# Kernel tuning notes

Hardware: AMD Instinct MI355X
Metric: run time of the kernel (lower is better)

The kernel has to match this reference:

```python
import jax, jax.numpy as jnp
import numpy as np
import math

N_EMBD = 1024
BATCH = 8
T = 2048
INIT_DECAY = 0.95


def setup_inputs() -> dict:
    key = jax.random.key(0)
    k1, k2 = jax.random.split(key)
    raw_init = math.log(INIT_DECAY / (1.0 - INIT_DECAY))
    x = jax.random.normal(k1, (BATCH, T, N_EMBD), dtype=jnp.float32)
    raw_a = jnp.full((N_EMBD,), raw_init, dtype=jnp.float32)
    B = jax.random.normal(k2, (N_EMBD, N_EMBD), dtype=jnp.float32) * 0.01
    h0 = jnp.zeros((BATCH, N_EMBD), dtype=jnp.float32)
    return {"x": x, "raw_a": raw_a, "B": B, "h0": h0}


def reference(x, raw_a, B, h0):
    # a: [H] diagonal decay in (0,1)
    a = jax.nn.sigmoid(raw_a)
    # Precompute the dense projection for all timesteps at once: u[b,t,h] = x[b,t,:] @ B.T
    u = jnp.einsum('btc,hc->bth', x, B)
    # Diagonal linear recurrence h_t = a * h_{t-1} + u_t via lax.scan over time.
    u_t_first = jnp.swapaxes(u, 0, 1)  # [T, B, H]

    def step(h, u_t):
        h = h * a + u_t
        return h, h

    _, ys = jax.lax.scan(step, h0, u_t_first)  # ys: [T, B, H]
    return jnp.swapaxes(ys, 0, 1)  # [B, T, H]
```

## Files before the change

kernel.cpp:

```cpp
#include <hip/hip_runtime.h>
#include <hip/hip_bf16.h>

using bf16 = __hip_bfloat16;
typedef __attribute__((ext_vector_type(8))) short frag8;
typedef __attribute__((ext_vector_type(4))) float f32x4;

constexpr int   H_   = 1024;
constexpr int   B_   = 8;
constexpr int   T_   = 2048;
constexpr int   K_   = H_;
constexpr int   N_   = H_;
constexpr long  M_   = (long)B_ * T_;
constexpr int   SEG  = 64;
constexpr int   TSEG = T_ / SEG;
constexpr int   NCH  = B_ * H_;
constexpr int   NVC  = NCH / 4;

__device__ __forceinline__ unsigned short f2bf(float f) {
  bf16 b = __float2bfloat16(f);
  return *reinterpret_cast<unsigned short*>(&b);
}

__device__ __forceinline__ float4 fma4(float4 h, float4 a, float4 v) {
  float4 r;
  r.x = fmaf(h.x, a.x, v.x);
  r.y = fmaf(h.y, a.y, v.y);
  r.z = fmaf(h.z, a.z, v.z);
  r.w = fmaf(h.w, a.w, v.w);
  return r;
}

__global__ __launch_bounds__(256) void k_convert(const float* __restrict__ x,
                                                 const float* __restrict__ Bm,
                                                 const float* __restrict__ raw,
                                                 unsigned short* __restrict__ xb,
                                                 unsigned short* __restrict__ Bb,
                                                 float* __restrict__ a_sig) {
  const long NX4 = (M_ * K_) / 4;
  const long NB4 = ((long)N_ * K_) / 4;
  long t = (long)blockIdx.x * 256 + threadIdx.x;
  const float* src; unsigned short* dst;
  if (t < NX4) { src = x; dst = xb; }
  else if (t < NX4 + NB4) { t -= NX4; src = Bm; dst = Bb; }
  else {
    long q = t - NX4 - NB4;
    if (q >= H_ / 4) return;
    float4 v = *reinterpret_cast<const float4*>(raw + q * 4);
    float4 o;
    o.x = 1.0f / (1.0f + expf(-v.x));
    o.y = 1.0f / (1.0f + expf(-v.y));
    o.z = 1.0f / (1.0f + expf(-v.z));
    o.w = 1.0f / (1.0f + expf(-v.w));
    *reinterpret_cast<float4*>(a_sig + q * 4) = o;
    return;
  }
  long i = t * 4;
  float4 v = *reinterpret_cast<const float4*>(src + i);
  short4 o;
  o.x = (short)f2bf(v.x);
  o.y = (short)f2bf(v.y);
  o.z = (short)f2bf(v.z);
  o.w = (short)f2bf(v.w);
  *reinterpret_cast<short4*>(dst + i) = o;
}

#define MEMBAR asm volatile("" ::: "memory")
#define BARR do { MEMBAR; __builtin_amdgcn_s_barrier(); MEMBAR; } while (0)
#define VMW(n) asm volatile("s_waitcnt vmcnt(" #n ")" ::: "memory")
#define GLDS(SRC, DST) __builtin_amdgcn_global_load_lds( \
    (const __attribute__((address_space(1))) void*)(SRC), \
    (__attribute__((address_space(3))) void*)(DST), 16, 0, 0)

__global__ __launch_bounds__(512, 2) void k_gemm(const unsigned short* __restrict__ A,
                                                 const unsigned short* __restrict__ Bb,
                                                 float* __restrict__ C,
                                                 const float* __restrict__ a_sig,
                                                 float* __restrict__ E) {
  __shared__ __align__(16) unsigned short lA[32768];
  __shared__ __align__(16) unsigned short lB[32768];
  const int tid  = threadIdx.x;
  const int wid  = tid >> 6, lane = tid & 63;
  const int wr   = wid >> 2, wc = wid & 3;
  const int quad = lane >> 4, l16 = lane & 15;
  const int sx   = l16 & 7;
  const int bh   = wc >> 1, br = (wc & 1) * 64;
  const int bid  = blockIdx.x;
  const int wgid = (bid & 7) * 32 + (bid >> 3);
  const long m0 = (long)(wgid >> 2) * 256;
  const long n0 = (long)(wgid & 3) * 256;
  const int sgran = (tid & 7) ^ ((tid >> 3) & 7);
  const unsigned short* gA = A  + (m0 + (tid >> 3)) * K_ + sgran * 8;
  const unsigned short* gB = Bb + (n0 + (tid >> 3)) * K_ + sgran * 8;
  unsigned short* sAw = lA + wid * 512;
  unsigned short* sBw = lB + wid * 512;

#define STG_A(d, hf, t) do { \
    GLDS(gA + ((hf) * 128) * K_ + (t) * 64,      sAw + (d) * 16384 + (hf) * 8192); \
    GLDS(gA + ((hf) * 128 + 64) * K_ + (t) * 64, sAw + (d) * 16384 + (hf) * 8192 + 4096); } while (0)
#define STG_B(d, hf, t) do { \
    GLDS(gB + ((hf) * 128) * K_ + (t) * 64,      sBw + (d) * 16384 + (hf) * 8192); \
    GLDS(gB + ((hf) * 128 + 64) * K_ + (t) * 64, sBw + (d) * 16384 + (hf) * 8192 + 4096); } while (0)

  f32x4 acc[8][4];
  #pragma unroll
  for (int i = 0; i < 8; i++)
    #pragma unroll
    for (int j = 0; j < 4; j++) acc[i][j] = f32x4{0.f, 0.f, 0.f, 0.f};

  frag8 aR[4][2];
  frag8 bR[2][2][2];

#define RD_A(d, ih) do { _Pragma("unroll") \
    for (int ii = 0; ii < 4; ii++) { \
      const unsigned short* rp = lA + (d) * 16384 + wr * 8192 + (((ih) * 4 + ii) * 16 + l16) * 64; \
      aR[ii][0] = *(const frag8*)(rp + (quad ^ sx) * 8); \
      aR[ii][1] = *(const frag8*)(rp + ((quad + 4) ^ sx) * 8); } } while (0)
#define RD_B(d, jh) do { _Pragma("unroll") \
    for (int jj = 0; jj < 2; jj++) { \
      const unsigned short* rp = lB + (d) * 16384 + bh * 8192 + (br + ((jh) * 2 + jj) * 16 + l16) * 64; \
      bR[jh][jj][0] = *(const frag8*)(rp + (quad ^ sx) * 8); \
      bR[jh][jj][1] = *(const frag8*)(rp + ((quad + 4) ^ sx) * 8); } } while (0)
#define MMQ(ih, jh) do { __builtin_amdgcn_s_setprio(1); _Pragma("unroll") \
    for (int ii = 0; ii < 4; ii++) { _Pragma("unroll") \
      for (int jj = 0; jj < 2; jj++) { \
        acc[(ih)*4+ii][(jh)*2+jj] = __builtin_amdgcn_mfma_f32_16x16x32_bf16(aR[ii][0], bR[jh][jj][0], acc[(ih)*4+ii][(jh)*2+jj], 0, 0, 0); \
        acc[(ih)*4+ii][(jh)*2+jj] = __builtin_amdgcn_mfma_f32_16x16x32_bf16(aR[ii][1], bR[jh][jj][1], acc[(ih)*4+ii][(jh)*2+jj], 0, 0, 0); } } \
    __builtin_amdgcn_s_setprio(0); } while (0)

  STG_A(0, 0, 0); STG_A(0, 1, 0); STG_B(0, 0, 0); STG_B(0, 1, 0); STG_A(1, 0, 1);
  VMW(2); BARR;

  for (int it = 0; it < 7; ++it) {
    const int to = 2 * it + 1, te2 = 2 * it + 2, to2 = 2 * it + 3;
    RD_A(0, 0); RD_B(0, 0); STG_A(1, 1, to);          BARR; MMQ(0, 0);
    RD_B(0, 1);             STG_B(1, 0, to);          BARR; MMQ(0, 1);
    RD_A(0, 1);             STG_B(1, 1, to);          BARR; MMQ(1, 1);
                            STG_A(0, 0, te2); VMW(2); BARR; MMQ(1, 0);
    RD_A(1, 0); RD_B(1, 0); STG_A(0, 1, te2);         BARR; MMQ(0, 0);
    RD_B(1, 1);             STG_B(0, 0, te2);         BARR; MMQ(0, 1);
    RD_A(1, 1);             STG_B(0, 1, te2);         BARR; MMQ(1, 1);
                            STG_A(1, 0, to2); VMW(2); BARR; MMQ(1, 0);
  }
  RD_A(0, 0); RD_B(0, 0); STG_A(1, 1, 15);         BARR; MMQ(0, 0);
  RD_B(0, 1);             STG_B(1, 0, 15);         BARR; MMQ(0, 1);
  RD_A(0, 1);             STG_B(1, 1, 15);         BARR; MMQ(1, 1);
                                           VMW(0); BARR; MMQ(1, 0);
  RD_A(1, 0); RD_B(1, 0);                          BARR; MMQ(0, 0);
  RD_B(1, 1);                                      BARR; MMQ(0, 1);
  RD_A(1, 1);                                      BARR; MMQ(1, 1);
  MMQ(1, 0);

  #pragma unroll
  for (int i = 0; i < 8; i++)
    #pragma unroll
    for (int j = 0; j < 4; j++) {
      const long r0 = m0 + wr * 128 + i * 16 + quad * 4;
      const long c0 = n0 + wc * 64 + j * 16 + l16;
      #pragma unroll
      for (int r = 0; r < 4; r++)
        C[(r0 + r) * N_ + c0] = acc[i][j][r];
    }

  {
    const int bb = (int)(m0 >> 11);
    const int sB = (int)((m0 & 2047) >> 5);
    #pragma unroll
    for (int j = 0; j < 4; j++) {
      const int c0 = (int)(n0) + wc * 64 + j * 16 + l16;
      const float a  = a_sig[c0];
      const float a2 = a * a, a4 = a2 * a2;
      float p4[8];
      p4[0] = 1.f;
      #pragma unroll
      for (int k = 1; k < 8; k++) p4[k] = p4[k - 1] * a4;
      #pragma unroll
      for (int sp = 0; sp < 4; sp++) {
        const f32x4 v = acc[sp * 2][j];
        const f32x4 w = acc[sp * 2 + 1][j];
        float p0 = ((v[0] * a + v[1]) * a + v[2]) * a + v[3];
        float p1 = ((w[0] * a + w[1]) * a + w[2]) * a + w[3];
        float e = p4[7 - quad] * p0 + p4[3 - quad] * p1;
        e += __shfl_xor(e, 16, 64);
        e += __shfl_xor(e, 32, 64);
        if (quad == 0) {
          const int sg = sB + wr * 4 + sp;
          E[(long)sg * NCH + bb * H_ + c0] = e;
        }
      }
    }
  }
}

__global__ __launch_bounds__(256) void k_scan(float* __restrict__ u,
                                              const float* __restrict__ E,
                                              const float* __restrict__ h0,
                                              const float* __restrict__ a_sig) {
  int g = blockIdx.x * 256 + threadIdx.x;
  int vc = g & (NVC - 1);
  int s  = g >> 11;
  int b  = vc >> 8;
  int h4 = (vc & 255) * 4;
  float4 a = *reinterpret_cast<const float4*>(a_sig + h4);
  float4 aL = a;
  #pragma unroll
  for (int i = 0; i < 5; i++) { aL.x *= aL.x; aL.y *= aL.y; aL.z *= aL.z; aL.w *= aL.w; }
  float4 hs = *reinterpret_cast<const float4*>(h0 + (long)vc * 4);
  int j = 0;
  for (; j + 8 <= s; j += 8) {
    float4 e[8];
    #pragma unroll
    for (int q = 0; q < 8; q++)
      e[q] = *reinterpret_cast<const float4*>(E + (long)(j + q) * NCH + (long)vc * 4);
    #pragma unroll
    for (int q = 0; q < 8; q++)
      hs = fma4(hs, aL, e[q]);
  }
  for (; j < s; ++j) {
    float4 e = *reinterpret_cast<const float4*>(E + (long)j * NCH + (long)vc * 4);
    hs = fma4(hs, aL, e);
  }

  float* base = u + (long)b * T_ * H_ + (long)s * TSEG * H_ + h4;

  float4 v0[8], v1[8];
  #pragma unroll
  for (int jj = 0; jj < 8; jj++)
    v0[jj] = *reinterpret_cast<const float4*>(base + (long)jj * H_);

  #pragma unroll
  for (int t0 = 0; t0 < TSEG; t0 += 8) {
    const bool odd = (t0 >> 3) & 1;
    float4* cur = odd ? v1 : v0;
    float4* nxt = odd ? v0 : v1;
    if (t0 + 8 < TSEG) {
      #pragma unroll
      for (int jj = 0; jj < 8; jj++)
        nxt[jj] = *reinterpret_cast<const float4*>(base + (long)(t0 + 8 + jj) * H_);
    }
    #pragma unroll
    for (int jj = 0; jj < 8; jj++) {
      hs = fma4(hs, a, cur[jj]);
      cur[jj] = hs;
    }
    #pragma unroll
    for (int jj = 0; jj < 8; jj++)
      *reinterpret_cast<float4*>(base + (long)(t0 + jj) * H_) = cur[jj];
  }
}

extern "C" void kernel_launch(void* const* d_in, const int* in_sizes, int n_in,
                              void* d_out, int out_size, void* d_ws, size_t ws_size,
                              hipStream_t stream) {
  const float* x    = (const float*)d_in[0];
  const float* rawa = (const float*)d_in[1];
  const float* Bm   = (const float*)d_in[2];
  const float* h0   = (const float*)d_in[3];
  float* u = (float*)d_out;

  char* w = (char*)d_ws;
  unsigned short* xb = (unsigned short*)w;
  unsigned short* Bb = (unsigned short*)(w + 33554432);
  float* a_sig = (float*)(w + 33554432 + 2097152);
  float* E     = (float*)(w + 33554432 + 2097152 + 4096);

  hipLaunchKernelGGL(k_convert, dim3(17409), dim3(256), 0, stream, x, Bm, rawa, xb, Bb, a_sig);
  hipLaunchKernelGGL(k_gemm, dim3(256), dim3(512), 0, stream, xb, Bb, u, a_sig, E);
  hipLaunchKernelGGL(k_scan, dim3(NVC * SEG / 256), dim3(256), 0, stream, u, E, h0, a_sig);
}
```

Measured before the change: 172.3 us.

## Store GEMM output as bf16 in workspace and scan from bf16 intermediate

The GEMM can now write the projection u as bf16 into a workspace buffer instead of fp32 into the output, and a new scan kernel reads those bf16 values, expands them to fp32 and writes the final states. This halves the intermediate write and read traffic between GEMM and scan, at the cost of bf16 rounding on u before the recurrence. The conversion kernel also processes 8 elements per thread with 16-byte stores. The bf16 path is used only when the workspace is large enough, otherwise the old fp32 path runs.

```diff
diff --git a/kernel.cpp b/kernel.cpp
--- a/kernel.cpp
+++ b/kernel.cpp
@@ -20,6 +20,10 @@
   bf16 b = __float2bfloat16(f);
   return *reinterpret_cast<unsigned short*>(&b);
 }
+__device__ __forceinline__ float bf2f(unsigned short u) {
+  unsigned v = (unsigned)u << 16;
+  return *reinterpret_cast<float*>(&v);
+}
 
 __device__ __forceinline__ float4 fma4(float4 h, float4 a, float4 v) {
   float4 r;
@@ -30,20 +34,21 @@
   return r;
 }
 
+typedef __attribute__((ext_vector_type(8))) short short8v;
 __global__ __launch_bounds__(256) void k_convert(const float* __restrict__ x,
                                                  const float* __restrict__ Bm,
                                                  const float* __restrict__ raw,
                                                  unsigned short* __restrict__ xb,
                                                  unsigned short* __restrict__ Bb,
                                                  float* __restrict__ a_sig) {
-  const long NX4 = (M_ * K_) / 4;
-  const long NB4 = ((long)N_ * K_) / 4;
+  const long NX8 = (M_ * K_) / 8;
+  const long NB8 = ((long)N_ * K_) / 8;
   long t = (long)blockIdx.x * 256 + threadIdx.x;
   const float* src; unsigned short* dst;
-  if (t < NX4) { src = x; dst = xb; }
-  else if (t < NX4 + NB4) { t -= NX4; src = Bm; dst = Bb; }
+  if (t < NX8) { src = x; dst = xb; }
+  else if (t < NX8 + NB8) { t -= NX8; src = Bm; dst = Bb; }
   else {
-    long q = t - NX4 - NB4;
+    long q = t - NX8 - NB8;
     if (q >= H_ / 4) return;
     float4 v = *reinterpret_cast<const float4*>(raw + q * 4);
     float4 o;
@@ -54,14 +59,15 @@
     *reinterpret_cast<float4*>(a_sig + q * 4) = o;
     return;
   }
-  long i = t * 4;
-  float4 v = *reinterpret_cast<const float4*>(src + i);
-  short4 o;
-  o.x = (short)f2bf(v.x);
-  o.y = (short)f2bf(v.y);
-  o.z = (short)f2bf(v.z);
-  o.w = (short)f2bf(v.w);
-  *reinterpret_cast<short4*>(dst + i) = o;
+  long i = t * 8;
+  float4 v0 = *reinterpret_cast<const float4*>(src + i);
+  float4 v1 = *reinterpret_cast<const float4*>(src + i + 4);
+  short8v o;
+  o[0] = (short)f2bf(v0.x); o[1] = (short)f2bf(v0.y);
+  o[2] = (short)f2bf(v0.z); o[3] = (short)f2bf(v0.w);
+  o[4] = (short)f2bf(v1.x); o[5] = (short)f2bf(v1.y);
+  o[6] = (short)f2bf(v1.z); o[7] = (short)f2bf(v1.w);
+  *reinterpret_cast<short8v*>(dst + i) = o;
 }
 
 #define MEMBAR asm volatile("" ::: "memory")
@@ -71,9 +77,11 @@
     (const __attribute__((address_space(1))) void*)(SRC), \
     (__attribute__((address_space(3))) void*)(DST), 16, 0, 0)
 
+template<int UBF>
 __global__ __launch_bounds__(512, 2) void k_gemm(const unsigned short* __restrict__ A,
                                                  const unsigned short* __restrict__ Bb,
                                                  float* __restrict__ C,
+                                                 unsigned short* __restrict__ UB,
                                                  const float* __restrict__ a_sig,
                                                  float* __restrict__ E) {
   __shared__ __align__(16) unsigned short lA[32768];
@@ -157,8 +165,10 @@
       const long r0 = m0 + wr * 128 + i * 16 + quad * 4;
       const long c0 = n0 + wc * 64 + j * 16 + l16;
       #pragma unroll
-      for (int r = 0; r < 4; r++)
-        C[(r0 + r) * N_ + c0] = acc[i][j][r];
+      for (int r = 0; r < 4; r++) {
+        if (UBF) UB[(r0 + r) * N_ + c0] = f2bf(acc[i][j][r]);
+        else     C [(r0 + r) * N_ + c0] = acc[i][j][r];
+      }
     }
 
   {
@@ -221,12 +231,10 @@
   }
 
   float* base = u + (long)b * T_ * H_ + (long)s * TSEG * H_ + h4;
-
   float4 v0[8], v1[8];
   #pragma unroll
   for (int jj = 0; jj < 8; jj++)
     v0[jj] = *reinterpret_cast<const float4*>(base + (long)jj * H_);
-
   #pragma unroll
   for (int t0 = 0; t0 < TSEG; t0 += 8) {
     const bool odd = (t0 >> 3) & 1;
@@ -245,6 +253,67 @@
     #pragma unroll
     for (int jj = 0; jj < 8; jj++)
       *reinterpret_cast<float4*>(base + (long)(t0 + jj) * H_) = cur[jj];
+  }
+}
+
+__global__ __launch_bounds__(256) void k_scan_bf(float* __restrict__ y,
+                                                 const unsigned short* __restrict__ ub,
+                                                 const float* __restrict__ E,
+                                                 const float* __restrict__ h0,
+                                                 const float* __restrict__ a_sig) {
+  int g = blockIdx.x * 256 + threadIdx.x;
+  int vc = g & (NVC - 1);
+  int s  = g >> 11;
+  int b  = vc >> 8;
+  int h4 = (vc & 255) * 4;
+  float4 a = *reinterpret_cast<const float4*>(a_sig + h4);
+  float4 aL = a;
+  #pragma unroll
+  for (int i = 0; i < 5; i++) { aL.x *= aL.x; aL.y *= aL.y; aL.z *= aL.z; aL.w *= aL.w; }
+  float4 hs = *reinterpret_cast<const float4*>(h0 + (long)vc * 4);
+  int j = 0;
+  for (; j + 8 <= s; j += 8) {
+    float4 e[8];
+    #pragma unroll
+    for (int q = 0; q < 8; q++)
+      e[q] = *reinterpret_cast<const float4*>(E + (long)(j + q) * NCH + (long)vc * 4);
+    #pragma unroll
+    for (int q = 0; q < 8; q++)
+      hs = fma4(hs, aL, e[q]);
+  }
+  for (; j < s; ++j) {
+    float4 e = *reinterpret_cast<const float4*>(E + (long)j * NCH + (long)vc * 4);
+    hs = fma4(hs, aL, e);
+  }
+
+  const long row0 = (long)b * T_ + (long)s * TSEG;
+  const unsigned short* ubase = ub + row0 * H_ + h4;
+  float* ybase = y + row0 * H_ + h4;
+
+  short4 v0[8], v1[8];
+  #pragma unroll
+  for (int jj = 0; jj < 8; jj++)
+    v0[jj] = *reinterpret_cast<const short4*>(ubase + (long)jj * H_);
+  #pragma unroll
+  for (int t0 = 0; t0 < TSEG; t0 += 8) {
+    const bool odd = (t0 >> 3) & 1;
+    short4* cur = odd ? v1 : v0;
+    short4* nxt = odd ? v0 : v1;
+    if (t0 + 8 < TSEG) {
+      #pragma unroll
+      for (int jj = 0; jj < 8; jj++)
+        nxt[jj] = *reinterpret_cast<const short4*>(ubase + (long)(t0 + 8 + jj) * H_);
+    }
+    #pragma unroll
+    for (int jj = 0; jj < 8; jj++) {
+      float4 v;
+      v.x = bf2f((unsigned short)cur[jj].x);
+      v.y = bf2f((unsigned short)cur[jj].y);
+      v.z = bf2f((unsigned short)cur[jj].z);
+      v.w = bf2f((unsigned short)cur[jj].w);
+      hs = fma4(hs, a, v);
+      *reinterpret_cast<float4*>(ybase + (long)(t0 + jj) * H_) = hs;
+    }
   }
 }
 
@@ -262,8 +331,19 @@
   unsigned short* Bb = (unsigned short*)(w + 33554432);
   float* a_sig = (float*)(w + 33554432 + 2097152);
   float* E     = (float*)(w + 33554432 + 2097152 + 4096);
-
-  hipLaunchKernelGGL(k_convert, dim3(17409), dim3(256), 0, stream, x, Bm, rawa, xb, Bb, a_sig);
-  hipLaunchKernelGGL(k_gemm, dim3(256), dim3(512), 0, stream, xb, Bb, u, a_sig, E);
-  hipLaunchKernelGGL(k_scan, dim3(NVC * SEG / 256), dim3(256), 0, stream, u, E, h0, a_sig);
-}
+  unsigned short* ub = (unsigned short*)(w + 37752832);
+  const bool big_ws = (ws_size >= (size_t)37752832 + 33554432);
+
+  hipLaunchKernelGGL(k_convert, dim3(8705), dim3(256), 0, stream, x, Bm, rawa, xb, Bb, a_sig);
+  if (big_ws) {
+    hipLaunchKernelGGL(HIP_KERNEL_NAME(k_gemm<1>), dim3(256), dim3(512), 0, stream,
+                       xb, Bb, u, ub, a_sig, E);
+    hipLaunchKernelGGL(k_scan_bf, dim3(NVC * SEG / 256), dim3(256), 0, stream,
+                       u, ub, E, h0, a_sig);
+  } else {
+    hipLaunchKernelGGL(HIP_KERNEL_NAME(k_gemm<0>), dim3(256), dim3(512), 0, stream,
+                       xb, Bb, u, ub, a_sig, E);
+    hipLaunchKernelGGL(k_scan, dim3(NVC * SEG / 256), dim3(256), 0, stream,
+                       u, E, h0, a_sig);
+  }
+}
```

Result: faster. 168.3 us (-2.3%).

## Fuse x bf16 conversion into GEMM loads and store u as bf16

Applied to the files above, without the earlier changes.

Removes the separate pass that converts x to bf16. The GEMM now loads fp32 x into registers, converts it, and writes bf16 into LDS inside the software pipeline, with adjusted vmcnt/lgkmcnt waits. The GEMM output u is also stored as bf16 in workspace, and the scan reads it and writes fp32 y to the output. This cuts the x-conversion round trip and halves the u write/read traffic, but adds register pressure, conversion ALU work inside the pipeline, and extra rounding of u to bf16.

```diff
diff --git a/kernel.cpp b/kernel.cpp
--- a/kernel.cpp
+++ b/kernel.cpp
@@ -3,6 +3,7 @@
 
 using bf16 = __hip_bfloat16;
 typedef __attribute__((ext_vector_type(8))) short frag8;
+typedef __attribute__((ext_vector_type(8))) short short8v;
 typedef __attribute__((ext_vector_type(4))) float f32x4;
 
 constexpr int   H_   = 1024;
@@ -20,6 +21,10 @@
   bf16 b = __float2bfloat16(f);
   return *reinterpret_cast<unsigned short*>(&b);
 }
+__device__ __forceinline__ float bf2f(unsigned short u) {
+  unsigned v = (unsigned)u << 16;
+  return *reinterpret_cast<float*>(&v);
+}
 
 __device__ __forceinline__ float4 fma4(float4 h, float4 a, float4 v) {
   float4 r;
@@ -30,50 +35,48 @@
   return r;
 }
 
-__global__ __launch_bounds__(256) void k_convert(const float* __restrict__ x,
-                                                 const float* __restrict__ Bm,
+__global__ __launch_bounds__(256) void k_convert(const float* __restrict__ Bm,
                                                  const float* __restrict__ raw,
-                                                 unsigned short* __restrict__ xb,
                                                  unsigned short* __restrict__ Bb,
                                                  float* __restrict__ a_sig) {
-  const long NX4 = (M_ * K_) / 4;
-  const long NB4 = ((long)N_ * K_) / 4;
+  const long NB8 = ((long)N_ * K_) / 8;
   long t = (long)blockIdx.x * 256 + threadIdx.x;
-  const float* src; unsigned short* dst;
-  if (t < NX4) { src = x; dst = xb; }
-  else if (t < NX4 + NB4) { t -= NX4; src = Bm; dst = Bb; }
-  else {
-    long q = t - NX4 - NB4;
-    if (q >= H_ / 4) return;
-    float4 v = *reinterpret_cast<const float4*>(raw + q * 4);
-    float4 o;
-    o.x = 1.0f / (1.0f + expf(-v.x));
-    o.y = 1.0f / (1.0f + expf(-v.y));
-    o.z = 1.0f / (1.0f + expf(-v.z));
-    o.w = 1.0f / (1.0f + expf(-v.w));
-    *reinterpret_cast<float4*>(a_sig + q * 4) = o;
+  if (t < NB8) {
+    long i = t * 8;
+    float4 v0 = *reinterpret_cast<const float4*>(Bm + i);
+    float4 v1 = *reinterpret_cast<const float4*>(Bm + i + 4);
+    short8v o;
+    o[0] = (short)f2bf(v0.x); o[1] = (short)f2bf(v0.y);
+    o[2] = (short)f2bf(v0.z); o[3] = (short)f2bf(v0.w);
+    o[4] = (short)f2bf(v1.x); o[5] = (short)f2bf(v1.y);
+    o[6] = (short)f2bf(v1.z); o[7] = (short)f2bf(v1.w);
+    *reinterpret_cast<short8v*>(Bb + i) = o;
     return;
   }
-  long i = t * 4;
-  float4 v = *reinterpret_cast<const float4*>(src + i);
-  short4 o;
-  o.x = (short)f2bf(v.x);
-  o.y = (short)f2bf(v.y);
-  o.z = (short)f2bf(v.z);
-  o.w = (short)f2bf(v.w);
-  *reinterpret_cast<short4*>(dst + i) = o;
+  long q = t - NB8;
+  if (q >= H_ / 4) return;
+  float4 v = *reinterpret_cast<const float4*>(raw + q * 4);
+  float4 o;
+  o.x = 1.0f / (1.0f + expf(-v.x));
+  o.y = 1.0f / (1.0f + expf(-v.y));
+  o.z = 1.0f / (1.0f + expf(-v.z));
+  o.w = 1.0f / (1.0f + expf(-v.w));
+  *reinterpret_cast<float4*>(a_sig + q * 4) = o;
 }
 
 #define MEMBAR asm volatile("" ::: "memory")
 #define BARR do { MEMBAR; __builtin_amdgcn_s_barrier(); MEMBAR; } while (0)
 #define VMW(n) asm volatile("s_waitcnt vmcnt(" #n ")" ::: "memory")
+#define LGKM0 asm volatile("s_waitcnt lgkmcnt(0)" ::: "memory")
 #define GLDS(SRC, DST) __builtin_amdgcn_global_load_lds( \
     (const __attribute__((address_space(1))) void*)(SRC), \
     (__attribute__((address_space(3))) void*)(DST), 16, 0, 0)
 
-__global__ __launch_bounds__(512, 2) void k_gemm(const unsigned short* __restrict__ A,
+struct ARegs { float4 f0, f1, f2, f3; };
+
+__global__ __launch_bounds__(512, 2) void k_gemm(const float* __restrict__ X,
                                                  const unsigned short* __restrict__ Bb,
-                                                 float* __restrict__ C,
+                                                 unsigned short* __restrict__ UB,
                                                  const float* __restrict__ a_sig,
                                                  float* __restrict__ E) {
   __shared__ __align__(16) unsigned short lA[32768];
@@ -89,14 +92,31 @@
   const long m0 = (long)(wgid >> 2) * 256;
   const long n0 = (long)(wgid & 3) * 256;
   const int sgran = (tid & 7) ^ ((tid >> 3) & 7);
-  const unsigned short* gA = A  + (m0 + (tid >> 3)) * K_ + sgran * 8;
+  const float*          gX = X  + (m0 + (tid >> 3)) * K_ + sgran * 8;
   const unsigned short* gB = Bb + (n0 + (tid >> 3)) * K_ + sgran * 8;
   unsigned short* sAw = lA + wid * 512;
   unsigned short* sBw = lB + wid * 512;
 
-#define STG_A(d, hf, t) do { \
-    GLDS(gA + ((hf) * 128) * K_ + (t) * 64,      sAw + (d) * 16384 + (hf) * 8192); \
-    GLDS(gA + ((hf) * 128 + 64) * K_ + (t) * 64, sAw + (d) * 16384 + (hf) * 8192 + 4096); } while (0)
+#define LD_A(dst, hf, t) do { \
+    const float* p0_ = gX + ((hf) * 128) * K_ + (t) * 64; \
+    const float* p1_ = gX + ((hf) * 128 + 64) * K_ + (t) * 64; \
+    dst.f0 = *reinterpret_cast<const float4*>(p0_); \
+    dst.f1 = *reinterpret_cast<const float4*>(p0_ + 4); \
+    dst.f2 = *reinterpret_cast<const float4*>(p1_); \
+    dst.f3 = *reinterpret_cast<const float4*>(p1_ + 4); } while (0)
+#define WR_A(d, hf, src) do { \
+    unsigned short* wp_ = sAw + (d) * 16384 + (hf) * 8192 + lane * 8; \
+    short8v o0_, o1_; \
+    o0_[0] = (short)f2bf(src.f0.x); o0_[1] = (short)f2bf(src.f0.y); \
+    o0_[2] = (short)f2bf(src.f0.z); o0_[3] = (short)f2bf(src.f0.w); \
+    o0_[4] = (short)f2bf(src.f1.x); o0_[5] = (short)f2bf(src.f1.y); \
+    o0_[6] = (short)f2bf(src.f1.z); o0_[7] = (short)f2bf(src.f1.w); \
+    o1_[0] = (short)f2bf(src.f2.x); o1_[1] = (short)f2bf(src.f2.y); \
+    o1_[2] = (short)f2bf(src.f2.z); o1_[3] = (short)f2bf(src.f2.w); \
+    o1_[4] = (short)f2bf(src.f3.x); o1_[5] = (short)f2bf(src.f3.y); \
+    o1_[6] = (short)f2bf(src.f3.z); o1_[7] = (short)f2bf(src.f3.w); \
+    *reinterpret_cast<short8v*>(wp_) = o0_; \
+    *reinterpret_cast<short8v*>(wp_ + 4096) = o1_; } while (0)
 #define STG_B(d, hf, t) do { \
     GLDS(gB + ((hf) * 128) * K_ + (t) * 64,      sBw + (d) * 16384 + (hf) * 8192); \
     GLDS(gB + ((hf) * 128 + 64) * K_ + (t) * 64, sBw + (d) * 16384 + (hf) * 8192 + 4096); } while (0)
@@ -109,6 +129,7 @@
 
   frag8 aR[4][2];
   frag8 bR[2][2][2];
+  ARegs aP, aQ, aRg, aS;
 
 #define RD_A(d, ih) do { _Pragma("unroll") \
     for (int ii = 0; ii < 4; ii++) { \
@@ -127,27 +148,33 @@
         acc[(ih)*4+ii][(jh)*2+jj] = __builtin_amdgcn_mfma_f32_16x16x32_bf16(aR[ii][1], bR[jh][jj][1], acc[(ih)*4+ii][(jh)*2+jj], 0, 0, 0); } } \
     __builtin_amdgcn_s_setprio(0); } while (0)
 
-  STG_A(0, 0, 0); STG_A(0, 1, 0); STG_B(0, 0, 0); STG_B(0, 1, 0); STG_A(1, 0, 1);
-  VMW(2); BARR;
+  LD_A(aQ, 0, 0); LD_A(aRg, 1, 0);
+  STG_B(0, 0, 0); STG_B(0, 1, 0);
+  LD_A(aS, 0, 1);
+  VMW(8);
+  WR_A(0, 0, aQ); WR_A(0, 1, aRg);
+  LGKM0;
+  VMW(4);
+  BARR;
 
   for (int it = 0; it < 7; ++it) {
     const int to = 2 * it + 1, te2 = 2 * it + 2, to2 = 2 * it + 3;
-    RD_A(0, 0); RD_B(0, 0); STG_A(1, 1, to);          BARR; MMQ(0, 0);
-    RD_B(0, 1);             STG_B(1, 0, to);          BARR; MMQ(0, 1);
-    RD_A(0, 1);             STG_B(1, 1, to);          BARR; MMQ(1, 1);
-                            STG_A(0, 0, te2); VMW(2); BARR; MMQ(1, 0);
-    RD_A(1, 0); RD_B(1, 0); STG_A(0, 1, te2);         BARR; MMQ(0, 0);
-    RD_B(1, 1);             STG_B(0, 0, te2);         BARR; MMQ(0, 1);
-    RD_A(1, 1);             STG_B(0, 1, te2);         BARR; MMQ(1, 1);
-                            STG_A(1, 0, to2); VMW(2); BARR; MMQ(1, 0);
-  }
-  RD_A(0, 0); RD_B(0, 0); STG_A(1, 1, 15);         BARR; MMQ(0, 0);
-  RD_B(0, 1);             STG_B(1, 0, 15);         BARR; MMQ(0, 1);
-  RD_A(0, 1);             STG_B(1, 1, 15);         BARR; MMQ(1, 1);
-                                           VMW(0); BARR; MMQ(1, 0);
-  RD_A(1, 0); RD_B(1, 0);                          BARR; MMQ(0, 0);
-  RD_B(1, 1);                                      BARR; MMQ(0, 1);
-  RD_A(1, 1);                                      BARR; MMQ(1, 1);
+    RD_A(0, 0); RD_B(0, 0); LD_A(aP, 1, to);                              BARR; MMQ(0, 0);
+    RD_B(0, 1); STG_B(1, 0, to);  VMW(6); WR_A(1, 0, aS);  LGKM0;         BARR; MMQ(0, 1);
+    RD_A(0, 1); STG_B(1, 1, to);  VMW(4); WR_A(1, 1, aP);  LGKM0;         BARR; MMQ(1, 1);
+                LD_A(aQ, 0, te2); VMW(4);                                 BARR; MMQ(1, 0);
+    RD_A(1, 0); RD_B(1, 0); LD_A(aRg, 1, te2);                            BARR; MMQ(0, 0);
+    RD_B(1, 1); STG_B(0, 0, te2); VMW(6); WR_A(0, 0, aQ);  LGKM0;         BARR; MMQ(0, 1);
+    RD_A(1, 1); STG_B(0, 1, te2); VMW(4); WR_A(0, 1, aRg); LGKM0;         BARR; MMQ(1, 1);
+                LD_A(aS, 0, to2); VMW(4);                                 BARR; MMQ(1, 0);
+  }
+  RD_A(0, 0); RD_B(0, 0); LD_A(aP, 1, 15);                                BARR; MMQ(0, 0);
+  RD_B(0, 1); STG_B(1, 0, 15); VMW(6); WR_A(1, 0, aS); LGKM0;             BARR; MMQ(0, 1);
+  RD_A(0, 1); STG_B(1, 1, 15); VMW(4); WR_A(1, 1, aP); LGKM0;             BARR; MMQ(1, 1);
+                               VMW(0);                                    BARR; MMQ(1, 0);
+  RD_A(1, 0); RD_B(1, 0);                                                 BARR; MMQ(0, 0);
+  RD_B(1, 1);                                                             BARR; MMQ(0, 1);
+  RD_A(1, 1);                                                             BARR; MMQ(1, 1);
   MMQ(1, 0);
 
   #pragma unroll
@@ -158,7 +185,7 @@
       const long c0 = n0 + wc * 64 + j * 16 + l16;
       #pragma unroll
       for (int r = 0; r < 4; r++)
-        C[(r0 + r) * N_ + c0] = acc[i][j][r];
+        UB[(r0 + r) * N_ + c0] = f2bf(acc[i][j][r]);
     }
 
   {
@@ -191,10 +218,11 @@
   }
 }
 
-__global__ __launch_bounds__(256) void k_scan(float* __restrict__ u,
-                                              const float* __restrict__ E,
-                                              const float* __restrict__ h0,
-                                              const float* __restrict__ a_sig) {
+__global__ __launch_bounds__(256) void k_scan_bf(float* __restrict__ y,
+                                                 const unsigned short* __restrict__ ub,
+                                                 const float* __restrict__ E,
+                                                 const float* __restrict__ h0,
+                                                 const float* __restrict__ a_sig) {
   int g = blockIdx.x * 256 + threadIdx.x;
   int vc = g & (NVC - 1);
   int s  = g >> 11;
@@ -220,31 +248,34 @@
     hs = fma4(hs, aL, e);
   }
 
-  float* base = u + (long)b * T_ * H_ + (long)s * TSEG * H_ + h4;
-
-  float4 v0[8], v1[8];
+  const long row0 = (long)b * T_ + (long)s * TSEG;
+  const unsigned short* ubase = ub + row0 * H_ + h4;
+  float* ybase = y + row0 * H_ + h4;
+
+  short4 v0[8], v1[8];
   #pragma unroll
   for (int jj = 0; jj < 8; jj++)
-    v0[jj] = *reinterpret_cast<const float4*>(base + (long)jj * H_);
-
+    v0[jj] = *reinterpret_cast<const short4*>(ubase + (long)jj * H_);
   #pragma unroll
   for (int t0 = 0; t0 < TSEG; t0 += 8) {
     const bool odd = (t0 >> 3) & 1;
-    float4* cur = odd ? v1 : v0;
-    float4* nxt = odd ? v0 : v1;
+    short4* cur = odd ? v1 : v0;
+    short4* nxt = odd ? v0 : v1;
     if (t0 + 8 < TSEG) {
       #pragma unroll
       for (int jj = 0; jj < 8; jj++)
-        nxt[jj] = *reinterpret_cast<const float4*>(base + (long)(t0 + 8 + jj) * H_);
+        nxt[jj] = *reinterpret_cast<const short4*>(ubase + (long)(t0 + 8 + jj) * H_);
     }
     #pragma unroll
     for (int jj = 0; jj < 8; jj++) {
-      hs = fma4(hs, a, cur[jj]);
-      cur[jj] = hs;
+      float4 v;
+      v.x = bf2f((unsigned short)cur[jj].x);
+      v.y = bf2f((unsigned short)cur[jj].y);
+      v.z = bf2f((unsigned short)cur[jj].z);
+      v.w = bf2f((unsigned short)cur[jj].w);
+      hs = fma4(hs, a, v);
+      *reinterpret_cast<float4*>(ybase + (long)(t0 + jj) * H_) = hs;
     }
-    #pragma unroll
-    for (int jj = 0; jj < 8; jj++)
-      *reinterpret_cast<float4*>(base + (long)(t0 + jj) * H_) = cur[jj];
   }
 }
 
@@ -255,15 +286,15 @@
   const float* rawa = (const float*)d_in[1];
   const float* Bm   = (const float*)d_in[2];
   const float* h0   = (const float*)d_in[3];
-  float* u = (float*)d_out;
+  float* y = (float*)d_out;
 
   char* w = (char*)d_ws;
-  unsigned short* xb = (unsigned short*)w;
   unsigned short* Bb = (unsigned short*)(w + 33554432);
   float* a_sig = (float*)(w + 33554432 + 2097152);
   float* E     = (float*)(w + 33554432 + 2097152 + 4096);
-
-  hipLaunchKernelGGL(k_convert, dim3(17409), dim3(256), 0, stream, x, Bm, rawa, xb, Bb, a_sig);
-  hipLaunchKernelGGL(k_gemm, dim3(256), dim3(512), 0, stream, xb, Bb, u, a_sig, E);
-  hipLaunchKernelGGL(k_scan, dim3(NVC * SEG / 256), dim3(256), 0, stream, u, E, h0, a_sig);
-}
+  unsigned short* ub = (unsigned short*)(w + 37752832);
+
+  hipLaunchKernelGGL(k_convert, dim3(513), dim3(256), 0, stream, Bm, rawa, Bb, a_sig);
+  hipLaunchKernelGGL(k_gemm, dim3(256), dim3(512), 0, stream, x, Bb, ub, a_sig, E);
+  hipLaunchKernelGGL(k_scan_bf, dim3(NVC * SEG / 256), dim3(256), 0, stream, y, ub, E, h0, a_sig);
+}
```

Result: no change. 173.9 us (+0.9%).
